# Performance work log

Hardware: AMD Instinct MI355X
Metric: run time of the kernel (lower is better)

Reference implementation:

```python
import jax, jax.numpy as jnp
import numpy as np

T = 100000


def setup_inputs() -> dict:
    key = jax.random.key(0)
    u = jax.random.normal(key, (1, T, 2), dtype=jnp.float32)
    M = jnp.array([20.0, 10.0], dtype=jnp.float32)
    C = jnp.array([10.0, 10.0, 10.0], dtype=jnp.float32)   # trainable damping
    K = jnp.array([2000.0, 1000.0, 5000.0], dtype=jnp.float32)
    x0 = jnp.zeros((1, 4), dtype=jnp.float32)              # [y1, v1, y2, v2]
    dt = jnp.asarray(0.002, dtype=jnp.float32)
    return {"u": u, "M": M, "C": C, "K": K, "x0": x0, "dt": dt}


def reference(u, M, C, K, x0, dt):
    # 2x2 coupled damping / stiffness matrices (same math as _fun)
    Cm = jnp.stack([jnp.stack([C[0] + C[1], -C[1]]),
                    jnp.stack([-C[1], C[2] + C[1]])])
    Km = jnp.stack([jnp.stack([K[0] + K[1], -K[1]]),
                    jnp.stack([-K[1], K[2] + K[1]])])

    def accel(z, v, ut):  # z, v, ut: [2]
        return (ut - Cm @ v - Km @ z) / M

    def step(carry, ut):
        y, v = carry
        k1 = accel(y, v, ut)
        y2 = y + v * (dt / 2.0); v2 = v + k1 * (dt / 2.0)
        k2 = accel(y2, v2, ut)
        y3 = y + v2 * (dt / 2.0); v3 = v + k2 * (dt / 2.0)
        k3 = accel(y3, v3, ut)
        y4 = y + v3 * dt; v4 = v + k3 * dt
        k4 = accel(y4, v4, ut)
        yn = y + (dt / 6.0) * (v + 2.0 * v2 + 2.0 * v3 + v4)
        vn = v + (dt / 6.0) * (k1 + 2.0 * k2 + 2.0 * k3 + k4)
        return (yn, vn), yn

    y0 = x0[0, ::2]   # positions [y1, y2]
    v0 = x0[0, 1::2]  # velocities [v1, v2]
    _, ys = jax.lax.scan(step, (y0, v0), u[0])  # ys: [T, 2]
    return ys[None]  # [1, T, 2] position sequence, matching RNN output y
```

## Files before the change

kernel.cpp:

```cpp
#include <hip/hip_runtime.h>


#define LSTEP  16
#define TPB    256
#define MAXNB  256

__device__ inline void accel_d(const double* M, const double* Cm, const double* Km,
                               const double* u, const double* z, const double* v, double* a) {
  a[0] = (u[0] - Cm[0] * v[0] - Cm[1] * v[1] - Km[0] * z[0] - Km[1] * z[1]) / M[0];
  a[1] = (u[1] - Cm[2] * v[0] - Cm[3] * v[1] - Km[2] * z[0] - Km[3] * z[1]) / M[1];
}

__device__ inline void rk4_step_d(const double* M, const double* Cm, const double* Km,
                                  double dt, double* y, double* v, const double* u) {
  double k1[2], k2[2], k3[2], k4[2];
  double y2[2], v2[2], y3[2], v3[2], y4[2], v4[2];
  double h = dt * 0.5;
  accel_d(M, Cm, Km, u, y, v, k1);
  y2[0] = y[0] + v[0] * h;  y2[1] = y[1] + v[1] * h;
  v2[0] = v[0] + k1[0] * h; v2[1] = v[1] + k1[1] * h;
  accel_d(M, Cm, Km, u, y2, v2, k2);
  y3[0] = y[0] + v2[0] * h;  y3[1] = y[1] + v2[1] * h;
  v3[0] = v[0] + k2[0] * h;  v3[1] = v[1] + k2[1] * h;
  accel_d(M, Cm, Km, u, y3, v3, k3);
  y4[0] = y[0] + v3[0] * dt; y4[1] = y[1] + v3[1] * dt;
  v4[0] = v[0] + k3[0] * dt; v4[1] = v[1] + k3[1] * dt;
  accel_d(M, Cm, Km, u, y4, v4, k4);
  double s = dt / 6.0;
  double yn0 = y[0] + s * (v[0] + 2.0 * v2[0] + 2.0 * v3[0] + v4[0]);
  double yn1 = y[1] + s * (v[1] + 2.0 * v2[1] + 2.0 * v3[1] + v4[1]);
  double vn0 = v[0] + s * (k1[0] + 2.0 * k2[0] + 2.0 * k3[0] + k4[0]);
  double vn1 = v[1] + s * (k1[1] + 2.0 * k2[1] + 2.0 * k3[1] + k4[1]);
  y[0] = yn0; y[1] = yn1; v[0] = vn0; v[1] = vn1;
}

__device__ inline void build_cols(const float* Mp, const float* Cp, const float* Kp,
                                  const float* dtp, float* Af, float* Bf, double* Ad) {
  int tid = threadIdx.x;
  if (tid < 6) {
    double M[2]  = {(double)Mp[0], (double)Mp[1]};
    double Cm[4] = {(double)Cp[0] + (double)Cp[1], -(double)Cp[1],
                    -(double)Cp[1], (double)Cp[2] + (double)Cp[1]};
    double Km[4] = {(double)Kp[0] + (double)Kp[1], -(double)Kp[1],
                    -(double)Kp[1], (double)Kp[2] + (double)Kp[1]};
    double dt = (double)dtp[0];
    double y[2] = {0, 0}, v[2] = {0, 0}, u[2] = {0, 0};
    if      (tid == 0) y[0] = 1.0;
    else if (tid == 1) y[1] = 1.0;
    else if (tid == 2) v[0] = 1.0;
    else if (tid == 3) v[1] = 1.0;
    else if (tid == 4) u[0] = 1.0;
    else               u[1] = 1.0;
    rk4_step_d(M, Cm, Km, dt, y, v, u);
    if (tid < 4) {
      if (Af) {
        Af[0 * 4 + tid] = (float)y[0]; Af[1 * 4 + tid] = (float)y[1];
        Af[2 * 4 + tid] = (float)v[0]; Af[3 * 4 + tid] = (float)v[1];
      }
      if (Ad) {
        Ad[0 * 4 + tid] = y[0]; Ad[1 * 4 + tid] = y[1];
        Ad[2 * 4 + tid] = v[0]; Ad[3 * 4 + tid] = v[1];
      }
    } else if (Bf) {
      int j = tid - 4;
      Bf[0 * 2 + j] = (float)y[0]; Bf[1 * 2 + j] = (float)y[1];
      Bf[2 * 2 + j] = (float)v[0]; Bf[3 * 2 + j] = (float)v[1];
    }
  }
}

__device__ inline float4 mv4(const float* A, float4 x) {
  float4 r;
  r.x = A[0]  * x.x + A[1]  * x.y + A[2]  * x.z + A[3]  * x.w;
  r.y = A[4]  * x.x + A[5]  * x.y + A[6]  * x.z + A[7]  * x.w;
  r.z = A[8]  * x.x + A[9]  * x.y + A[10] * x.z + A[11] * x.w;
  r.w = A[12] * x.x + A[13] * x.y + A[14] * x.z + A[15] * x.w;
  return r;
}
__device__ inline float4 f4add(float4 a, float4 b) {
  return make_float4(a.x + b.x, a.y + b.y, a.z + b.z, a.w + b.w);
}
__device__ inline float4 stepf(const float* a, const float* b, float4 s, float2 ut) {
  float4 r;
  r.x = a[0]  * s.x + a[1]  * s.y + a[2]  * s.z + a[3]  * s.w + b[0] * ut.x + b[1] * ut.y;
  r.y = a[4]  * s.x + a[5]  * s.y + a[6]  * s.z + a[7]  * s.w + b[2] * ut.x + b[3] * ut.y;
  r.z = a[8]  * s.x + a[9]  * s.y + a[10] * s.z + a[11] * s.w + b[4] * ut.x + b[5] * ut.y;
  r.w = a[12] * s.x + a[13] * s.y + a[14] * s.z + a[15] * s.w + b[6] * ut.x + b[7] * ut.y;
  return r;
}

__device__ inline double matmul16(double a, double b, int i, int j) {
  double acc = 0.0;
#pragma unroll
  for (int k = 0; k < 4; ++k)
    acc += __shfl(a, i * 4 + k) * __shfl(b, k * 4 + j);
  return acc;
}

__global__ __launch_bounds__(TPB) void kFused(
    const float* __restrict__ u, const float* M, const float* C, const float* K,
    const float* dtp, const float* x0, int T,
    float4* __restrict__ agg, int* __restrict__ flags, float2* __restrict__ out) {
  __shared__ float  Af[16], Bf[8];
  __shared__ double Ad[16];
  __shared__ float  Wlev[8][16];
  __shared__ float  Wf[16];
  __shared__ float4 S[TPB];
  __shared__ float4 sB;

  int tid = threadIdx.x;
  int b   = blockIdx.x;

  build_cols(M, C, K, dtp, Af, Bf, Ad);
  __syncthreads();

  if (tid < 16) {
    int i = tid >> 2, jj = tid & 3;
    double m = Ad[tid];
#pragma unroll
    for (int l = 0; l < 4; ++l) m = matmul16(m, m, i, jj);
    Wlev[0][tid] = (float)m;
#pragma unroll
    for (int k = 1; k < 8; ++k) { m = matmul16(m, m, i, jj); Wlev[k][tid] = (float)m; }
    m = matmul16(m, m, i, jj);
    Wf[tid] = (float)m;
  }
  __syncthreads();

  float a[16], bb[8];
#pragma unroll
  for (int e = 0; e < 16; ++e) a[e] = Af[e];
#pragma unroll
  for (int e = 0; e < 8; ++e) bb[e] = Bf[e];

  int j  = b * TPB + tid;
  int t0 = j * LSTEP;
  bool full = (t0 + LSTEP <= T);
  float4 uu[LSTEP / 2];
  float4 c = make_float4(0.f, 0.f, 0.f, 0.f);
  if (full) {
    const float4* u4 = (const float4*)(u + 2 * t0);
#pragma unroll
    for (int i = 0; i < LSTEP / 2; ++i) uu[i] = u4[i];
#pragma unroll
    for (int i = 0; i < LSTEP / 2; ++i) {
      c = stepf(a, bb, c, make_float2(uu[i].x, uu[i].y));
      c = stepf(a, bb, c, make_float2(uu[i].z, uu[i].w));
    }
  } else {
    const float2* u2 = (const float2*)u;
    for (int i = 0; i < LSTEP; ++i) {
      int t = t0 + i;
      if (t >= T) break;
      c = stepf(a, bb, c, u2[t]);
    }
  }

  S[tid] = c;
  __syncthreads();
#pragma unroll
  for (int k = 0; k < 8; ++k) {
    int off = 1 << k;
    float4 add = make_float4(0.f, 0.f, 0.f, 0.f);
    bool act = (tid >= off);
    if (act) add = mv4(&Wlev[k][0], S[tid - off]);
    __syncthreads();
    if (act) S[tid] = f4add(S[tid], add);
    __syncthreads();
  }
  float4 E = (tid == 0) ? make_float4(0.f, 0.f, 0.f, 0.f) : S[tid - 1];

  if (tid == 0) {
    float4 s0v = make_float4(x0[0], x0[2], x0[1], x0[3]);
    float4 o = S[TPB - 1];
    if (b == 0) o = f4add(mv4(Wf, s0v), o);
    agg[b] = o;
    __threadfence();
    __hip_atomic_store(&flags[b], 1, __ATOMIC_RELEASE, __HIP_MEMORY_SCOPE_AGENT);

    float4 acc;
    if (b == 0) {
      acc = s0v;
    } else {
      acc = make_float4(0.f, 0.f, 0.f, 0.f);
      float Wk[16], Wl[16], t[16];
#pragma unroll
      for (int e = 0; e < 16; ++e) { Wk[e] = ((e & 5) == 0 && (e >> 2) == (e & 3)) ? 1.f : 0.f; }
#pragma unroll
      for (int e = 0; e < 16; ++e) { Wk[e] = ((e >> 2) == (e & 3)) ? 1.f : 0.f; Wl[e] = Wf[e]; }
      for (int p = b - 1; p >= 0; --p) {
        while (__hip_atomic_load(&flags[p], __ATOMIC_ACQUIRE, __HIP_MEMORY_SCOPE_AGENT) != 1) {}
        float4 op = agg[p];
        acc = f4add(acc, mv4(Wk, op));
        if (p > 0) {
#pragma unroll
          for (int i2 = 0; i2 < 4; ++i2)
#pragma unroll
            for (int j2 = 0; j2 < 4; ++j2)
              t[i2 * 4 + j2] = Wk[i2 * 4 + 0] * Wl[0 * 4 + j2] + Wk[i2 * 4 + 1] * Wl[1 * 4 + j2]
                             + Wk[i2 * 4 + 2] * Wl[2 * 4 + j2] + Wk[i2 * 4 + 3] * Wl[3 * 4 + j2];
#pragma unroll
          for (int e = 0; e < 16; ++e) Wk[e] = t[e];
        }
      }
    }
    sB = acc;
  }
  __syncthreads();

  S[tid] = (tid == 0) ? sB : make_float4(0.f, 0.f, 0.f, 0.f);
  __syncthreads();
#pragma unroll
  for (int k = 0; k < 8; ++k) {
    int off = 1 << k;
    float4 add = make_float4(0.f, 0.f, 0.f, 0.f);
    bool act = (tid >= off);
    if (act) add = mv4(&Wlev[k][0], S[tid - off]);
    __syncthreads();
    if (act) S[tid] = f4add(S[tid], add);
    __syncthreads();
  }
  float4 st = f4add(S[tid], E);

  if (full) {
    float4* o4 = (float4*)(out + t0);
#pragma unroll
    for (int i = 0; i < LSTEP / 2; ++i) {
      st = stepf(a, bb, st, make_float2(uu[i].x, uu[i].y));
      float2 ya = make_float2(st.x, st.y);
      st = stepf(a, bb, st, make_float2(uu[i].z, uu[i].w));
      o4[i] = make_float4(ya.x, ya.y, st.x, st.y);
    }
  } else {
    const float2* u2 = (const float2*)u;
    for (int i = 0; i < LSTEP; ++i) {
      int t = t0 + i;
      if (t >= T) break;
      st = stepf(a, bb, st, u2[t]);
      out[t] = make_float2(st.x, st.y);
    }
  }
}

__global__ void kSerialAll(const float* u, const float* Mp, const float* Cp, const float* Kp,
                           const float* dtp, const float* x0, int T, float2* out) {
  if (threadIdx.x != 0 || blockIdx.x != 0) return;
  double M[2]  = {(double)Mp[0], (double)Mp[1]};
  double Cm[4] = {(double)Cp[0] + (double)Cp[1], -(double)Cp[1],
                  -(double)Cp[1], (double)Cp[2] + (double)Cp[1]};
  double Km[4] = {(double)Kp[0] + (double)Kp[1], -(double)Kp[1],
                  -(double)Kp[1], (double)Kp[2] + (double)Kp[1]};
  double dt = (double)dtp[0];
  double y[2] = {(double)x0[0], (double)x0[2]};
  double v[2] = {(double)x0[1], (double)x0[3]};
  for (int t = 0; t < T; ++t) {
    double uu[2] = {(double)u[2 * t], (double)u[2 * t + 1]};
    rk4_step_d(M, Cm, Km, dt, y, v, uu);
    out[t] = make_float2((float)y[0], (float)y[1]);
  }
}

extern "C" void kernel_launch(void* const* d_in, const int* in_sizes, int n_in,
                              void* d_out, int out_size, void* d_ws, size_t ws_size,
                              hipStream_t stream) {
  (void)n_in; (void)out_size;
  const float* u   = (const float*)d_in[0];
  const float* M   = (const float*)d_in[1];
  const float* C   = (const float*)d_in[2];
  const float* K   = (const float*)d_in[3];
  const float* x0  = (const float*)d_in[4];
  const float* dt  = (const float*)d_in[5];
  int T = in_sizes[0] / 2;
  float2* out = (float2*)d_out;

  int nch = (T + LSTEP - 1) / LSTEP;
  int nb  = (nch + TPB - 1) / TPB;
  size_t need = (size_t)MAXNB * (sizeof(float4) + sizeof(int));
  if (nb > MAXNB || ws_size < need) {
    kSerialAll<<<1, 64, 0, stream>>>(u, M, C, K, dt, x0, T, out);
    return;
  }
  float4* agg  = (float4*)d_ws;
  int* flags   = (int*)(agg + MAXNB);
  kFused<<<nb, TPB, 0, stream>>>(u, M, C, K, dt, x0, T, agg, flags, out);
}
```

Baseline: 81.22 us.

## Precompute power tables and parallelize cross-block carry with wave reduction

Builds shared-memory tables of transition-matrix powers: a per-thread table for chunk offsets 0..255 and a per-block table for block offsets 0..24. The serial per-block look-back loop run by thread 0, which did a 4x4 matrix multiply per predecessor, becomes a parallel gather. Each lane waits on one predecessor's flag, applies the precomputed power, and the results are summed with a wave shuffle reduction. The second 8-level scan that propagated the block carry is replaced by one matrix-vector multiply per thread, and the input loads are hoisted ahead of the setup work. In exchange it adds table-building work and a larger shared-memory footprint, and it caps the fused path at 64 blocks, though the power table only covers block offsets up to 24.

```diff
diff --git a/kernel.cpp b/kernel.cpp
--- a/kernel.cpp
+++ b/kernel.cpp
@@ -53,15 +53,11 @@
     else               u[1] = 1.0;
     rk4_step_d(M, Cm, Km, dt, y, v, u);
     if (tid < 4) {
-      if (Af) {
-        Af[0 * 4 + tid] = (float)y[0]; Af[1 * 4 + tid] = (float)y[1];
-        Af[2 * 4 + tid] = (float)v[0]; Af[3 * 4 + tid] = (float)v[1];
-      }
-      if (Ad) {
-        Ad[0 * 4 + tid] = y[0]; Ad[1 * 4 + tid] = y[1];
-        Ad[2 * 4 + tid] = v[0]; Ad[3 * 4 + tid] = v[1];
-      }
-    } else if (Bf) {
+      Af[0 * 4 + tid] = (float)y[0]; Af[1 * 4 + tid] = (float)y[1];
+      Af[2 * 4 + tid] = (float)v[0]; Af[3 * 4 + tid] = (float)v[1];
+      Ad[0 * 4 + tid] = y[0]; Ad[1 * 4 + tid] = y[1];
+      Ad[2 * 4 + tid] = v[0]; Ad[3 * 4 + tid] = v[1];
+    } else {
       int j = tid - 4;
       Bf[0 * 2 + j] = (float)y[0]; Bf[1 * 2 + j] = (float)y[1];
       Bf[2 * 2 + j] = (float)v[0]; Bf[3 * 2 + j] = (float)v[1];
@@ -88,6 +84,14 @@
   r.w = a[12] * s.x + a[13] * s.y + a[14] * s.z + a[15] * s.w + b[6] * ut.x + b[7] * ut.y;
   return r;
 }
+__device__ inline void mm4(const float* X, const float* Y, float* Z) {
+#pragma unroll
+  for (int i = 0; i < 4; ++i)
+#pragma unroll
+    for (int j = 0; j < 4; ++j)
+      Z[i * 4 + j] = X[i * 4 + 0] * Y[0 * 4 + j] + X[i * 4 + 1] * Y[1 * 4 + j]
+                   + X[i * 4 + 2] * Y[2 * 4 + j] + X[i * 4 + 3] * Y[3 * 4 + j];
+}
 
 __device__ inline double matmul16(double a, double b, int i, int j) {
   double acc = 0.0;
@@ -103,45 +107,67 @@
     float4* __restrict__ agg, int* __restrict__ flags, float2* __restrict__ out) {
   __shared__ float  Af[16], Bf[8];
   __shared__ double Ad[16];
-  __shared__ float  Wlev[8][16];
-  __shared__ float  Wf[16];
+  __shared__ float  Tt[256][16];
+  __shared__ float  Wt[32][16];
   __shared__ float4 S[TPB];
-  __shared__ float4 sB;
+  __shared__ float4 sBsh;
 
   int tid = threadIdx.x;
   int b   = blockIdx.x;
-
-  build_cols(M, C, K, dtp, Af, Bf, Ad);
-  __syncthreads();
-
-  if (tid < 16) {
-    int i = tid >> 2, jj = tid & 3;
-    double m = Ad[tid];
-#pragma unroll
-    for (int l = 0; l < 4; ++l) m = matmul16(m, m, i, jj);
-    Wlev[0][tid] = (float)m;
-#pragma unroll
-    for (int k = 1; k < 8; ++k) { m = matmul16(m, m, i, jj); Wlev[k][tid] = (float)m; }
-    m = matmul16(m, m, i, jj);
-    Wf[tid] = (float)m;
-  }
-  __syncthreads();
-
-  float a[16], bb[8];
-#pragma unroll
-  for (int e = 0; e < 16; ++e) a[e] = Af[e];
-#pragma unroll
-  for (int e = 0; e < 8; ++e) bb[e] = Bf[e];
 
   int j  = b * TPB + tid;
   int t0 = j * LSTEP;
   bool full = (t0 + LSTEP <= T);
   float4 uu[LSTEP / 2];
+  if (full) {
+    const float4* u4 = (const float4*)(u + 2 * t0);
+#pragma unroll
+    for (int i = 0; i < LSTEP / 2; ++i) uu[i] = u4[i];
+  }
+
+  build_cols(M, C, K, dtp, Af, Bf, Ad);
+  if (tid == 0) {
+#pragma unroll
+    for (int e = 0; e < 16; ++e) {
+      float v = ((e >> 2) == (e & 3)) ? 1.f : 0.f;
+      Tt[0][e] = v; Wt[0][e] = v;
+    }
+  }
+  __syncthreads();
+
+  if (tid < 16) {
+    int i = tid >> 2, jj = tid & 3;
+    double m = Ad[tid];
+#pragma unroll
+    for (int lvl = 1; lvl <= 16; ++lvl) {
+      m = matmul16(m, m, i, jj);
+      if (lvl >= 4 && lvl <= 11) Tt[1 << (lvl - 4)][tid] = (float)m;
+      if (lvl >= 12)             Wt[1 << (lvl - 12)][tid] = (float)m;
+    }
+  }
+  __syncthreads();
+
+#pragma unroll
+  for (int d = 1; d < 8; ++d) {
+    int off = 1 << d;
+    if (tid > off && tid < 2 * off)
+      mm4(&Tt[tid - off][0], &Tt[off][0], &Tt[tid][0]);
+    if (d <= 4) {
+      int k = tid - 128;
+      if (k > off && k < 2 * off && k < 25 && tid >= 128 + off + 1)
+        mm4(&Wt[k - off][0], &Wt[off][0], &Wt[k][0]);
+    }
+    __syncthreads();
+  }
+
+  float a[16], bb[8];
+#pragma unroll
+  for (int e = 0; e < 16; ++e) a[e] = Af[e];
+#pragma unroll
+  for (int e = 0; e < 8; ++e) bb[e] = Bf[e];
+
   float4 c = make_float4(0.f, 0.f, 0.f, 0.f);
   if (full) {
-    const float4* u4 = (const float4*)(u + 2 * t0);
-#pragma unroll
-    for (int i = 0; i < LSTEP / 2; ++i) uu[i] = u4[i];
 #pragma unroll
     for (int i = 0; i < LSTEP / 2; ++i) {
       c = stepf(a, bb, c, make_float2(uu[i].x, uu[i].y));
@@ -163,64 +189,46 @@
     int off = 1 << k;
     float4 add = make_float4(0.f, 0.f, 0.f, 0.f);
     bool act = (tid >= off);
-    if (act) add = mv4(&Wlev[k][0], S[tid - off]);
+    if (act) add = mv4(&Tt[off][0], S[tid - off]);
     __syncthreads();
     if (act) S[tid] = f4add(S[tid], add);
     __syncthreads();
   }
   float4 E = (tid == 0) ? make_float4(0.f, 0.f, 0.f, 0.f) : S[tid - 1];
 
+  float4 s0v = make_float4(x0[0], x0[2], x0[1], x0[3]);
   if (tid == 0) {
-    float4 s0v = make_float4(x0[0], x0[2], x0[1], x0[3]);
     float4 o = S[TPB - 1];
-    if (b == 0) o = f4add(mv4(Wf, s0v), o);
+    if (b == 0) o = f4add(mv4(&Wt[1][0], s0v), o);
     agg[b] = o;
     __threadfence();
     __hip_atomic_store(&flags[b], 1, __ATOMIC_RELEASE, __HIP_MEMORY_SCOPE_AGENT);
-
-    float4 acc;
-    if (b == 0) {
-      acc = s0v;
-    } else {
-      acc = make_float4(0.f, 0.f, 0.f, 0.f);
-      float Wk[16], Wl[16], t[16];
-#pragma unroll
-      for (int e = 0; e < 16; ++e) { Wk[e] = ((e & 5) == 0 && (e >> 2) == (e & 3)) ? 1.f : 0.f; }
-#pragma unroll
-      for (int e = 0; e < 16; ++e) { Wk[e] = ((e >> 2) == (e & 3)) ? 1.f : 0.f; Wl[e] = Wf[e]; }
-      for (int p = b - 1; p >= 0; --p) {
+  }
+  float4 sB;
+  if (b == 0) {
+    sB = s0v;
+  } else {
+    if (tid < 64) {
+      float4 acc = make_float4(0.f, 0.f, 0.f, 0.f);
+      if (tid < b) {
+        int p = tid;
         while (__hip_atomic_load(&flags[p], __ATOMIC_ACQUIRE, __HIP_MEMORY_SCOPE_AGENT) != 1) {}
-        float4 op = agg[p];
-        acc = f4add(acc, mv4(Wk, op));
-        if (p > 0) {
-#pragma unroll
-          for (int i2 = 0; i2 < 4; ++i2)
-#pragma unroll
-            for (int j2 = 0; j2 < 4; ++j2)
-              t[i2 * 4 + j2] = Wk[i2 * 4 + 0] * Wl[0 * 4 + j2] + Wk[i2 * 4 + 1] * Wl[1 * 4 + j2]
-                             + Wk[i2 * 4 + 2] * Wl[2 * 4 + j2] + Wk[i2 * 4 + 3] * Wl[3 * 4 + j2];
-#pragma unroll
-          for (int e = 0; e < 16; ++e) Wk[e] = t[e];
-        }
+        acc = mv4(&Wt[b - 1 - p][0], agg[p]);
       }
-    }
-    sB = acc;
-  }
-  __syncthreads();
-
-  S[tid] = (tid == 0) ? sB : make_float4(0.f, 0.f, 0.f, 0.f);
-  __syncthreads();
-#pragma unroll
-  for (int k = 0; k < 8; ++k) {
-    int off = 1 << k;
-    float4 add = make_float4(0.f, 0.f, 0.f, 0.f);
-    bool act = (tid >= off);
-    if (act) add = mv4(&Wlev[k][0], S[tid - off]);
-    __syncthreads();
-    if (act) S[tid] = f4add(S[tid], add);
-    __syncthreads();
-  }
-  float4 st = f4add(S[tid], E);
+#pragma unroll
+      for (int o2 = 32; o2 >= 1; o2 >>= 1) {
+        acc.x += __shfl_xor(acc.x, o2);
+        acc.y += __shfl_xor(acc.y, o2);
+        acc.z += __shfl_xor(acc.z, o2);
+        acc.w += __shfl_xor(acc.w, o2);
+      }
+      if (tid == 0) sBsh = acc;
+    }
+    __syncthreads();
+    sB = sBsh;
+  }
+
+  float4 st = f4add(mv4(&Tt[tid][0], sB), E);
 
   if (full) {
     float4* o4 = (float4*)(out + t0);
@@ -276,7 +284,7 @@
   int nch = (T + LSTEP - 1) / LSTEP;
   int nb  = (nch + TPB - 1) / TPB;
   size_t need = (size_t)MAXNB * (sizeof(float4) + sizeof(int));
-  if (nb > MAXNB || ws_size < need) {
+  if (nb > 64 || ws_size < need) {
     kSerialAll<<<1, 64, 0, stream>>>(u, M, C, K, dt, x0, T, out);
     return;
   }
```

New measurement: 76.49 us. -5.8%, faster.
